# Optimization experiments

Hardware: AMD Instinct MI355X
Metric: run time of the kernel (lower is better)

## Reference

```python
import jax, jax.numpy as jnp
import numpy as np
import math

B, T, C, H = 2, 2048, 1024, 16
D = C // H  # head dim 64

def setup_inputs() -> dict:
    key = jax.random.key(0)
    ks = jax.random.split(key, 3)
    scale = 0.02
    return {
        "x": jax.random.normal(ks[0], (B, T, C), dtype=jnp.float32),
        "W_attn": jax.random.normal(ks[1], (C, 3 * C), dtype=jnp.float32) * scale,
        "b_attn": jnp.zeros((3 * C,), dtype=jnp.float32),
        "W_proj": jax.random.normal(ks[2], (C, C), dtype=jnp.float32) * scale,
        "b_proj": jnp.zeros((C,), dtype=jnp.float32),
    }

def reference(x, W_attn, b_attn, W_proj, b_proj):
    Bb, Tt, Cc = x.shape
    qkv = x @ W_attn + b_attn                       # [B,T,3C]
    q, k, v = jnp.split(qkv, 3, axis=-1)
    # [B,T,C] -> [B,H,T,D]
    def heads(t):
        return t.reshape(Bb, Tt, H, D).transpose(0, 2, 1, 3)
    q, k, v = heads(q), heads(k), heads(v)
    scores = jnp.einsum('bhqd,bhkd->bhqk', q, k) * (1.0 / math.sqrt(D))
    causal = jnp.tril(jnp.ones((Tt, Tt), dtype=bool))
    scores = jnp.where(causal, scores, -jnp.inf)
    attn = jax.nn.softmax(scores, axis=-1)
    out = jnp.einsum('bhqk,bhkd->bhqd', attn, v)    # [B,H,T,D]
    out = out.transpose(0, 2, 1, 3).reshape(Bb, Tt, Cc)
    return out @ W_proj + b_proj
```

## Files before the change

kernel.cpp:

```cpp
#include <hip/hip_runtime.h>

typedef unsigned short u16;
typedef unsigned int u32;
typedef float f32x4 __attribute__((ext_vector_type(4)));
typedef float f32x16 __attribute__((ext_vector_type(16)));
typedef unsigned int u32x4 __attribute__((ext_vector_type(4)));
typedef unsigned int u32x2 __attribute__((ext_vector_type(2)));
typedef unsigned short u16x8 __attribute__((ext_vector_type(8)));
typedef unsigned short u16x4 __attribute__((ext_vector_type(4)));

#define DEV static __device__ __forceinline__

constexpr int BB = 2, TT = 2048, CC = 1024, HH = 16, DD = 64;
constexpr int MDIM = BB * TT;

DEV u16 f2bf(float f) {
  unsigned int u = __builtin_bit_cast(unsigned int, f);
  u += 0x7fffu + ((u >> 16) & 1u);
  return (u16)(u >> 16);
}
DEV float bf2f(u16 h) {
  unsigned int u = ((unsigned int)h) << 16;
  return __builtin_bit_cast(float, u);
}
DEV void async16(const void* g, void* l) {
  __builtin_amdgcn_global_load_lds(
      (const __attribute__((address_space(1))) unsigned int*)g,
      (__attribute__((address_space(3))) unsigned int*)l, 16, 0, 0);
}
DEV void mfma16(f32x4& acc, u32x4 a, u32x4 b) {
  asm volatile("v_mfma_f32_16x16x32_bf16 %0, %1, %2, %0"
               : "+v"(acc)
               : "v"(a), "v"(b));
}
DEV void mfma32(f32x16& acc, u32x4 a, u32x4 b) {
  asm volatile("v_mfma_f32_32x32x16_bf16 %0, %1, %2, %0"
               : "+v"(acc)
               : "v"(a), "v"(b));
}
DEV u32 cvtpk(float lo, float hi) {
  u32 r;
  asm("v_cvt_pk_bf16_f32 %0, %1, %2" : "=v"(r) : "v"(lo), "v"(hi));
  return r;
}
DEV void pswap(u32& a, u32& b) {
#if __has_builtin(__builtin_amdgcn_permlane32_swap)
  u32x2 r = __builtin_amdgcn_permlane32_swap(a, b, false, false);
  a = r.x;
  b = r.y;
#else
  asm volatile("v_permlane32_swap_b32 %0, %1" : "+v"(a), "+v"(b));
#endif
}
DEV float exp2g(float x) {
#if __has_builtin(__builtin_amdgcn_exp2f)
  return __builtin_amdgcn_exp2f(x);
#else
  return exp2f(x);
#endif
}

__global__ void prep_all(const float* __restrict__ x,
                         const float* __restrict__ Wa, const float* __restrict__ Wp,
                         u16* __restrict__ x_bf,
                         u16* __restrict__ Wa_t, u16* __restrict__ Wp_t) {
  __shared__ float tile[32][33];
  int bx = blockIdx.x;
  const int tx = threadIdx.x, ty = threadIdx.y;
  if (bx >= 128) {
    const int cb = (bx - 128) * 32 + blockIdx.y;
    const int i = (cb * 1024 + ty * 32 + tx) * 4;
    f32x4 v = *(const f32x4*)(x + i);
    u16x4 o;
#pragma unroll
    for (int j = 0; j < 4; ++j) o[j] = f2bf(v[j]);
    *(u16x4*)(x_bf + i) = o;
    return;
  }
  const float* in;
  u16* out;
  int Cc;
  if (bx < 96) { in = Wa; out = Wa_t; Cc = 3072; }
  else { bx -= 96; in = Wp; out = Wp_t; Cc = 1024; }
  const int R = 1024;
  const int x0 = bx * 32, y0 = blockIdx.y * 32;
  tile[ty][tx] = in[(size_t)(y0 + ty) * Cc + (x0 + tx)];
  __syncthreads();
  out[(size_t)(x0 + ty) * R + (y0 + tx)] = f2bf(tile[tx][ty]);
}

__global__ __launch_bounds__(512, 2) void gemm_qkv256(
    const u16* __restrict__ A, const u16* __restrict__ Bt,
    const float* __restrict__ bias,
    u16* __restrict__ qw, u16* __restrict__ kw, u16* __restrict__ vw) {
  extern __shared__ char smem[];
  const int K = CC, NT = K / 64;
  const int tid = threadIdx.x;
  const int lane = tid & 63, w = tid >> 6;
  const int g = lane >> 4, c16 = lane & 15;
  const int wm2 = (w >> 2) * 128, wn2 = (w & 3) * 48;

  const int wgid = blockIdx.x;
  const int xcd = wgid & 7, idx = wgid >> 3;
  const int patch = xcd * 2 + (idx >> 4);
  const int q = idx & 15;
  const int bys = (patch & 3) * 4 + (q & 3);
  const int bxs = (patch >> 2) * 4 + (q >> 2);
  const int brow = bys * 256, bcol = bxs * 192;

  const int lrow = lane >> 3;
  const int scol = ((lane & 7) ^ lrow) << 4;
  const int rswz = (c16 & 7) << 4;

  f32x4 acc[8][3];
#pragma unroll
  for (int m = 0; m < 8; ++m)
#pragma unroll
    for (int n = 0; n < 3; ++n) acc[m][n] = f32x4{0.f, 0.f, 0.f, 0.f};

  const size_t ldb = (size_t)K * 2;
  const char* Abase = (const char*)A + (size_t)brow * ldb;
  const char* Bbase = (const char*)Bt + (size_t)bcol * ldb;

  auto STAGE = [&](int kt) {
    const int par = kt & 1;
    char* Adst = smem + par * 32768;
    char* Bdst = smem + 65536 + par * 24576;
    const size_t koff = (size_t)kt * 128;
#pragma unroll
    for (int i = 0; i < 4; ++i) {
      const int c = w * 4 + i;
      const int row = c * 8 + lrow;
      async16(Abase + (size_t)row * ldb + koff + scol, Adst + c * 1024);
    }
#pragma unroll
    for (int i = 0; i < 3; ++i) {
      const int c = w * 3 + i;
      const int row = c * 8 + lrow;
      async16(Bbase + (size_t)row * ldb + koff + scol, Bdst + c * 1024);
    }
  };

  STAGE(0);
  STAGE(1);

  for (int kt = 0; kt < NT; ++kt) {
    const int par = kt & 1;
    if (kt + 1 < NT)
      asm volatile("s_waitcnt vmcnt(7)" ::: "memory");
    else
      asm volatile("s_waitcnt vmcnt(0)" ::: "memory");
    __builtin_amdgcn_sched_barrier(0);
    __builtin_amdgcn_s_barrier();
    __builtin_amdgcn_sched_barrier(0);
    const char* Ap = smem + par * 32768;
    const char* Bp = smem + 65536 + par * 24576;
#pragma unroll
    for (int kc = 0; kc < 2; ++kc) {
      const int cb = (kc * 64 + g * 16) ^ rswz;
      u32x4 af[8], bf[3];
#pragma unroll
      for (int m = 0; m < 8; ++m)
        af[m] = *(const u32x4*)(Ap + (wm2 + m * 16 + c16) * 128 + cb);
#pragma unroll
      for (int n = 0; n < 3; ++n)
        bf[n] = *(const u32x4*)(Bp + (wn2 + n * 16 + c16) * 128 + cb);
      asm volatile("s_waitcnt lgkmcnt(0)" ::: "memory");
      __builtin_amdgcn_sched_barrier(0);
      __builtin_amdgcn_s_setprio(1);
#pragma unroll
      for (int m = 0; m < 8; ++m)
#pragma unroll
        for (int n = 0; n < 3; ++n) mfma16(acc[m][n], af[m], bf[n]);
      __builtin_amdgcn_s_setprio(0);
    }
    __builtin_amdgcn_s_barrier();
    if (kt + 2 < NT) STAGE(kt + 2);
  }

  u16* E = (u16*)smem;
#pragma unroll
  for (int n = 0; n < 3; ++n) {
    const float bv = bias[bcol + wn2 + n * 16 + c16];
#pragma unroll
    for (int m = 0; m < 8; ++m)
#pragma unroll
      for (int r = 0; r < 4; ++r)
        E[(wm2 + m * 16 + g * 4 + r) * 192 + wn2 + n * 16 + c16] =
            f2bf(acc[m][n][r] + bv);
  }
  __syncthreads();
#pragma unroll
  for (int i = 0; i < 12; ++i) {
    const int c = tid + i * 512;
    {
      const int row = c / 24, col8 = (c % 24) * 8;
      const int colg = bcol + col8;
      if (colg < 2048) {
        const int which = colg >> 10, cc = colg & 1023, h = cc >> 6, d = cc & 63;
        const int rowg = brow + row, b = rowg >> 11, t = rowg & (TT - 1);
        u16x8 v8 = *(const u16x8*)&E[row * 192 + col8];
        u16* dst = (which == 0 ? qw : kw) + ((size_t)(b * HH + h) * TT + t) * DD + d;
        *(u16x8*)dst = v8;
      }
    }
    {
      const int col = c % 192, row8 = (c / 192) * 8;
      const int colg = bcol + col;
      if (colg >= 2048) {
        const int cc = colg & 1023, h = cc >> 6, d = cc & 63;
        const int rowg = brow + row8, b = rowg >> 11, t = rowg & (TT - 1);
        u16x8 v8;
#pragma unroll
        for (int j = 0; j < 8; ++j) v8[j] = E[(row8 + j) * 192 + col];
        u16* dst = vw + ((size_t)(b * HH + h) * DD + d) * TT + t;
        *(u16x8*)dst = v8;
      }
    }
  }
}

__global__ __launch_bounds__(256) void gemm_proj(
    const u16* __restrict__ A, const u16* __restrict__ Bt,
    const float* __restrict__ bias, float* __restrict__ outF,
    int M, int N, int K) {
  __shared__ alignas(16) u16 Sh[2][128 * 64];
  u16* Asp = Sh[0];
  u16* Bsp = Sh[1];
  const int tid = threadIdx.x;
  const int lane = tid & 63, w = tid >> 6;
  const int g = lane >> 4, c16 = lane & 15;
  const int wm = (w >> 1) * 64, wn = (w & 1) * 64;

  const int wgid = blockIdx.y * gridDim.x + blockIdx.x;
  const int xcd = wgid & 7, pi = wgid >> 3;
  const int bxs = pi & 7;
  const int bys = 4 * xcd + (pi >> 3);
  const int brow = bys * 128, bcol = bxs * 128;

  const int lrow = lane >> 3;
  const int scol = ((lane & 7) ^ lrow) << 4;
  const int rswz = (c16 & 7) << 4;

  f32x4 acc[4][4];
#pragma unroll
  for (int m = 0; m < 4; ++m)
#pragma unroll
    for (int n = 0; n < 4; ++n) acc[m][n] = f32x4{0.f, 0.f, 0.f, 0.f};

  const size_t ldb = (size_t)K * 2;
  const char* Abase = (const char*)A + (size_t)brow * ldb;
  const char* Bbase = (const char*)Bt + (size_t)bcol * ldb;

  for (int kt = 0; kt < K; kt += 64) {
    __syncthreads();
#pragma unroll
    for (int i = 0; i < 4; ++i) {
      const int chunk = i * 4 + w;
      const int row = chunk * 8 + lrow;
      async16(Abase + (size_t)row * ldb + (size_t)kt * 2 + scol, (char*)Asp + chunk * 1024);
      async16(Bbase + (size_t)row * ldb + (size_t)kt * 2 + scol, (char*)Bsp + chunk * 1024);
    }
    __syncthreads();
#pragma unroll
    for (int kc = 0; kc < 2; ++kc) {
      const int cb = (kc * 64 + g * 16) ^ rswz;
      u32x4 af[4], bf8[4];
#pragma unroll
      for (int m = 0; m < 4; ++m)
        af[m] = *(const u32x4*)((const char*)Asp + (wm + m * 16 + c16) * 128 + cb);
#pragma unroll
      for (int n = 0; n < 4; ++n)
        bf8[n] = *(const u32x4*)((const char*)Bsp + (wn + n * 16 + c16) * 128 + cb);
#pragma unroll
      for (int m = 0; m < 4; ++m)
#pragma unroll
        for (int n = 0; n < 4; ++n) mfma16(acc[m][n], af[m], bf8[n]);
    }
  }

  float* Ef = (float*)&Sh[0][0];
#pragma unroll
  for (int pass = 0; pass < 2; ++pass) {
    __syncthreads();
    if ((wm >> 6) == pass) {
#pragma unroll
      for (int n = 0; n < 4; ++n) {
        const float bv = bias[bcol + wn + n * 16 + c16];
#pragma unroll
        for (int m = 0; m < 4; ++m)
#pragma unroll
          for (int r = 0; r < 4; ++r)
            Ef[(m * 16 + g * 4 + r) * 128 + wn + n * 16 + c16] = acc[m][n][r] + bv;
      }
    }
    __syncthreads();
#pragma unroll
    for (int i = 0; i < 8; ++i) {
      const int chunk = tid + i * 256;
      const int row = chunk >> 5;
      const int c4 = (chunk & 31) * 4;
      f32x4 v4 = *(const f32x4*)&Ef[row * 128 + c4];
      *(f32x4*)&outF[(size_t)(brow + pass * 64 + row) * N + bcol + c4] = v4;
    }
  }
}

__global__ __launch_bounds__(256) void attn_fwd(
    const u16* __restrict__ qw, const u16* __restrict__ kw,
    const u16* __restrict__ vw, u16* __restrict__ ao) {
  extern __shared__ u16 smem_a[];
  const int tid = threadIdx.x;
  const int lane = tid & 63, w = tid >> 6;
  const int ql = lane & 31, half = lane >> 5;
  const int bh = blockIdx.y;
  const int qb = ((bh >> 4) & 1) ? (15 - blockIdx.x) : blockIdx.x;
  const int q0w = qb * 128 + w * 32;
  const int qg = q0w + ql;
  const int lrow = lane >> 3;
  const int scol = ((lane & 7) ^ lrow) << 4;
  const int rswz = (ql & 7) << 4;

  u32x4 qf[4];
  {
    const u16* qrow = qw + ((size_t)bh * TT + qg) * DD;
    const float qs = 0.125f * 1.44269504f;
#pragma unroll
    for (int dwin = 0; dwin < 4; ++dwin) {
      u16x8 u = *(const u16x8*)(qrow + dwin * 16 + half * 8);
      u16x8 s;
#pragma unroll
      for (int j = 0; j < 8; ++j) s[j] = f2bf(bf2f(u[j]) * qs);
      qf[dwin] = __builtin_bit_cast(u32x4, s);
    }
  }

  f32x16 o0, o1;
#pragma unroll
  for (int i = 0; i < 16; ++i) { o0[i] = 0.f; o1[i] = 0.f; }
  float l_run = 0.f;

  const char* kbase = (const char*)kw + ((size_t)bh * TT) * 128;
  const char* vbase = (const char*)vw + ((size_t)bh * DD) * (TT * 2);

  const int nt = 2 * qb + 2;

  auto kptr = [&](int b) { return (char*)(smem_a + (b & 3) * 4096); };
  auto vptr = [&](int b) { return (char*)(smem_a + 16384 + (b & 3) * 4096); };

  auto STAGE = [&](int kt_) {
    if (kt_ >= nt) return;
    const int t0_ = kt_ * 64;
#pragma unroll
    for (int i_ = 0; i_ < 2; ++i_) {
      const int chunk = w * 2 + i_;
      const int row = chunk * 8 + lrow;
      async16(kbase + (size_t)(t0_ + row) * 128 + scol, kptr(kt_) + chunk * 1024);
      async16(vbase + (size_t)row * (TT * 2) + (size_t)t0_ * 2 + scol,
              vptr(kt_) + chunk * 1024);
    }
  };

  auto QK = [&](int kt_, f32x16& sa, f32x16& sb) {
    const char* Kc = kptr(kt_);
#pragma unroll
    for (int i = 0; i < 16; ++i) { sa[i] = 0.f; sb[i] = 0.f; }
    __builtin_amdgcn_s_setprio(1);
#pragma unroll
    for (int dwin = 0; dwin < 4; ++dwin) {
      const int cb = (dwin * 32 + half * 16) ^ rswz;
      u32x4 ak0 = *(const u32x4*)(Kc + (0 + ql) * 128 + cb);
      u32x4 ak1 = *(const u32x4*)(Kc + (32 + ql) * 128 + cb);
      mfma32(sa, ak0, qf[dwin]);
      mfma32(sb, ak1, qf[dwin]);
    }
    __builtin_amdgcn_s_setprio(0);
  };

  auto FINISH = [&](int kt_, f32x16& s0, f32x16& s1) {
    const int t0 = kt_ * 64;
    if (t0 >= q0w + 32) return;
    if (t0 + 63 > q0w) {
      const int kb = t0 + 4 * half - qg;
#pragma unroll
      for (int r = 0; r < 16; ++r) {
        const int ko = (r & 3) + 8 * (r >> 2);
        if (kb + ko > 0) s0[r] = -1e30f;
        if (kb + 32 + ko > 0) s1[r] = -1e30f;
      }
    }
#pragma unroll
    for (int i = 0; i < 16; ++i) {
      s0[i] = exp2g(s0[i]);
      s1[i] = exp2g(s1[i]);
    }
    float a8[8];
#pragma unroll
    for (int i = 0; i < 8; ++i)
      a8[i] = (s0[i] + s0[i + 8]) + (s1[i] + s1[i + 8]);
    float rs = ((a8[0] + a8[1]) + (a8[2] + a8[3])) + ((a8[4] + a8[5]) + (a8[6] + a8[7]));
    rs += __shfl_xor(rs, 32, 64);
    l_run += rs;

    u32x4 pf[4];
#pragma unroll
    for (int win = 0; win < 4; ++win) {
      const int b = (win & 1) * 8;
      u32 w0, w1, w2, w3;
      if (win < 2) {
        w0 = cvtpk(s0[b + 0], s0[b + 1]); w2 = cvtpk(s0[b + 4], s0[b + 5]);
        w1 = cvtpk(s0[b + 2], s0[b + 3]); w3 = cvtpk(s0[b + 6], s0[b + 7]);
      } else {
        w0 = cvtpk(s1[b + 0], s1[b + 1]); w2 = cvtpk(s1[b + 4], s1[b + 5]);
        w1 = cvtpk(s1[b + 2], s1[b + 3]); w3 = cvtpk(s1[b + 6], s1[b + 7]);
      }
      pswap(w0, w2);
      pswap(w1, w3);
      pf[win] = u32x4{w0, w1, w2, w3};
    }
    const char* Vc = vptr(kt_);
    __builtin_amdgcn_s_setprio(1);
#pragma unroll
    for (int win = 0; win < 4; ++win) {
      const int cb = (win * 32 + half * 16) ^ rswz;
      u32x4 av0 = *(const u32x4*)(Vc + (0 + ql) * 128 + cb);
      u32x4 av1 = *(const u32x4*)(Vc + (32 + ql) * 128 + cb);
      mfma32(o0, av0, pf[win]);
      mfma32(o1, av1, pf[win]);
    }
    __builtin_amdgcn_s_setprio(0);
  };

  STAGE(0);
  STAGE(1);
  STAGE(2);
  if (nt >= 3)
    asm volatile("s_waitcnt vmcnt(8)" ::: "memory");
  else
    asm volatile("s_waitcnt vmcnt(4)" ::: "memory");
  __builtin_amdgcn_sched_barrier(0);
  __builtin_amdgcn_s_barrier();
  __builtin_amdgcn_sched_barrier(0);

  f32x16 sA0, sA1, sB0, sB1;
  QK(0, sA0, sA1);

#define BODY(KT, C0, C1, N0, N1)                                          \
  {                                                                       \
    const int kt_b = (KT);                                                \
    if (kt_b + 2 < nt)                                                    \
      asm volatile("s_waitcnt vmcnt(4)" ::: "memory");                    \
    else                                                                  \
      asm volatile("s_waitcnt vmcnt(0)" ::: "memory");                    \
    __builtin_amdgcn_sched_barrier(0);                                    \
    __builtin_amdgcn_s_barrier();                                         \
    __builtin_amdgcn_sched_barrier(0);                                    \
    STAGE(kt_b + 3);                                                      \
    if (kt_b + 1 < nt && (kt_b + 1) * 64 < q0w + 32) QK(kt_b + 1, N0, N1);\
    FINISH(kt_b, C0, C1);                                                 \
  }

  for (int kt2 = 0; kt2 < nt; kt2 += 2) {
    BODY(kt2, sA0, sA1, sB0, sB1);
    BODY(kt2 + 1, sB0, sB1, sA0, sA1);
  }
#undef BODY

  const int b = bh >> 4, h = bh & 15;
  const float inv = 1.f / l_run;
  u16* aorow = ao + ((size_t)(b * TT) + qg) * CC + h * DD;
#pragma unroll
  for (int rg = 0; rg < 4; ++rg) {
    u16x4 t0v, t1v;
#pragma unroll
    for (int j = 0; j < 4; ++j) {
      t0v[j] = f2bf(o0[rg * 4 + j] * inv);
      t1v[j] = f2bf(o1[rg * 4 + j] * inv);
    }
    *(u16x4*)(aorow + 8 * rg + 4 * half) = t0v;
    *(u16x4*)(aorow + 32 + 8 * rg + 4 * half) = t1v;
  }
}

extern "C" void kernel_launch(void* const* d_in, const int* in_sizes, int n_in,
                              void* d_out, int out_size, void* d_ws, size_t ws_size,
                              hipStream_t stream) {
  const float* x  = (const float*)d_in[0];
  const float* Wa = (const float*)d_in[1];
  const float* ba = (const float*)d_in[2];
  const float* Wp = (const float*)d_in[3];
  const float* bp = (const float*)d_in[4];
  float* out = (float*)d_out;

  char* ws = (char*)d_ws;
  const size_t MB = 1ull << 20;
  u16* x_bf = (u16*)(ws);
  u16* ao   = (u16*)(ws);
  u16* Wa_t = (u16*)(ws + 8 * MB);
  u16* Wp_t = (u16*)(ws + 14 * MB);
  u16* q_ws = (u16*)(ws + 16 * MB);
  u16* k_ws = (u16*)(ws + 24 * MB);
  u16* v_ws = (u16*)(ws + 32 * MB);

  static bool attr_set = []() {
    hipFuncSetAttribute((const void*)gemm_qkv256,
                        hipFuncAttributeMaxDynamicSharedMemorySize, 114688);
    hipFuncSetAttribute((const void*)attn_fwd,
                        hipFuncAttributeMaxDynamicSharedMemorySize, 65536);
    return true;
  }();
  (void)attr_set;

  hipLaunchKernelGGL(prep_all, dim3(160, 32), dim3(32, 32), 0, stream,
                     x, Wa, Wp, x_bf, Wa_t, Wp_t);
  hipLaunchKernelGGL(gemm_qkv256, dim3(256), dim3(512), 114688, stream,
                     x_bf, Wa_t, ba, q_ws, k_ws, v_ws);
  hipLaunchKernelGGL(attn_fwd, dim3(TT / 128, BB * HH), dim3(256), 65536, stream,
                     q_ws, k_ws, v_ws, ao);
  hipLaunchKernelGGL(gemm_proj, dim3(CC / 128, MDIM / 128), dim3(256), 0, stream,
                     ao, Wp_t, bp, out, MDIM, CC, CC);
}
```

Baseline: 108.0 us.

## Switch attention to 16x16 MFMA tiles with 8 waves per block

The attention kernel moves from 32x32x16 MFMA with 32 query rows per wave to 16x16x32 MFMA with 16 query rows per wave, and doubles the block to 512 threads (8 waves) covering the same 128 query rows. The P operand is rearranged with ds_bpermute instead of permlane32 swaps, and each wave now stages a single K/V chunk, so the vmcnt thresholds are halved. The aim is more waves per CU and finer causal-mask granularity for better latency hiding. The cost is extra LDS bpermute traffic, more K/V LDS reads per query, and the lower throughput per instruction of the smaller MFMA shape.

```diff
diff --git a/kernel.cpp b/kernel.cpp
--- a/kernel.cpp
+++ b/kernel.cpp
@@ -33,24 +33,10 @@
                : "+v"(acc)
                : "v"(a), "v"(b));
 }
-DEV void mfma32(f32x16& acc, u32x4 a, u32x4 b) {
-  asm volatile("v_mfma_f32_32x32x16_bf16 %0, %1, %2, %0"
-               : "+v"(acc)
-               : "v"(a), "v"(b));
-}
 DEV u32 cvtpk(float lo, float hi) {
   u32 r;
   asm("v_cvt_pk_bf16_f32 %0, %1, %2" : "=v"(r) : "v"(lo), "v"(hi));
   return r;
-}
-DEV void pswap(u32& a, u32& b) {
-#if __has_builtin(__builtin_amdgcn_permlane32_swap)
-  u32x2 r = __builtin_amdgcn_permlane32_swap(a, b, false, false);
-  a = r.x;
-  b = r.y;
-#else
-  asm volatile("v_permlane32_swap_b32 %0, %1" : "+v"(a), "+v"(b));
-#endif
 }
 DEV float exp2g(float x) {
 #if __has_builtin(__builtin_amdgcn_exp2f)
@@ -306,38 +292,40 @@
   }
 }
 
-__global__ __launch_bounds__(256) void attn_fwd(
+__global__ __launch_bounds__(512) void attn_fwd(
     const u16* __restrict__ qw, const u16* __restrict__ kw,
     const u16* __restrict__ vw, u16* __restrict__ ao) {
   extern __shared__ u16 smem_a[];
   const int tid = threadIdx.x;
   const int lane = tid & 63, w = tid >> 6;
-  const int ql = lane & 31, half = lane >> 5;
+  const int q16 = lane & 15, g = lane >> 4;
   const int bh = blockIdx.y;
   const int qb = ((bh >> 4) & 1) ? (15 - blockIdx.x) : blockIdx.x;
-  const int q0w = qb * 128 + w * 32;
-  const int qg = q0w + ql;
+  const int q0w = qb * 128 + w * 16;
+  const int qg = q0w + q16;
   const int lrow = lane >> 3;
   const int scol = ((lane & 7) ^ lrow) << 4;
-  const int rswz = (ql & 7) << 4;
-
-  u32x4 qf[4];
+  const int rswz = (q16 & 7) << 4;
+  const int addr0 = (q16 + 32 * (g & 1)) * 4;
+  const int addr1 = addr0 + 64;
+
+  u32x4 qf[2];
   {
     const u16* qrow = qw + ((size_t)bh * TT + qg) * DD;
     const float qs = 0.125f * 1.44269504f;
 #pragma unroll
-    for (int dwin = 0; dwin < 4; ++dwin) {
-      u16x8 u = *(const u16x8*)(qrow + dwin * 16 + half * 8);
+    for (int kc = 0; kc < 2; ++kc) {
+      u16x8 u = *(const u16x8*)(qrow + kc * 32 + g * 8);
       u16x8 s;
 #pragma unroll
       for (int j = 0; j < 8; ++j) s[j] = f2bf(bf2f(u[j]) * qs);
-      qf[dwin] = __builtin_bit_cast(u32x4, s);
-    }
-  }
-
-  f32x16 o0, o1;
-#pragma unroll
-  for (int i = 0; i < 16; ++i) { o0[i] = 0.f; o1[i] = 0.f; }
+      qf[kc] = __builtin_bit_cast(u32x4, s);
+    }
+  }
+
+  f32x4 o[4];
+#pragma unroll
+  for (int df = 0; df < 4; ++df) o[df] = f32x4{0.f, 0.f, 0.f, 0.f};
   float l_run = 0.f;
 
   const char* kbase = (const char*)kw + ((size_t)bh * TT) * 128;
@@ -351,118 +339,116 @@
   auto STAGE = [&](int kt_) {
     if (kt_ >= nt) return;
     const int t0_ = kt_ * 64;
-#pragma unroll
-    for (int i_ = 0; i_ < 2; ++i_) {
-      const int chunk = w * 2 + i_;
-      const int row = chunk * 8 + lrow;
-      async16(kbase + (size_t)(t0_ + row) * 128 + scol, kptr(kt_) + chunk * 1024);
-      async16(vbase + (size_t)row * (TT * 2) + (size_t)t0_ * 2 + scol,
-              vptr(kt_) + chunk * 1024);
-    }
+    const int row = w * 8 + lrow;
+    async16(kbase + (size_t)(t0_ + row) * 128 + scol, kptr(kt_) + w * 1024);
+    async16(vbase + (size_t)row * (TT * 2) + (size_t)t0_ * 2 + scol,
+            vptr(kt_) + w * 1024);
   };
 
-  auto QK = [&](int kt_, f32x16& sa, f32x16& sb) {
+  auto QK = [&](int kt_, f32x4* sa) {
+#pragma unroll
+    for (int kf = 0; kf < 4; ++kf) sa[kf] = f32x4{0.f, 0.f, 0.f, 0.f};
     const char* Kc = kptr(kt_);
-#pragma unroll
-    for (int i = 0; i < 16; ++i) { sa[i] = 0.f; sb[i] = 0.f; }
     __builtin_amdgcn_s_setprio(1);
 #pragma unroll
-    for (int dwin = 0; dwin < 4; ++dwin) {
-      const int cb = (dwin * 32 + half * 16) ^ rswz;
-      u32x4 ak0 = *(const u32x4*)(Kc + (0 + ql) * 128 + cb);
-      u32x4 ak1 = *(const u32x4*)(Kc + (32 + ql) * 128 + cb);
-      mfma32(sa, ak0, qf[dwin]);
-      mfma32(sb, ak1, qf[dwin]);
+    for (int kc = 0; kc < 2; ++kc) {
+      const int cb = (kc * 64 + g * 16) ^ rswz;
+#pragma unroll
+      for (int kf = 0; kf < 4; ++kf) {
+        u32x4 ak = *(const u32x4*)(Kc + (kf * 16 + q16) * 128 + cb);
+        mfma16(sa[kf], ak, qf[kc]);
+      }
     }
     __builtin_amdgcn_s_setprio(0);
   };
 
-  auto FINISH = [&](int kt_, f32x16& s0, f32x16& s1) {
+  auto FINISH = [&](int kt_, f32x4* s) {
     const int t0 = kt_ * 64;
-    if (t0 >= q0w + 32) return;
+    if (t0 >= q0w + 16) return;
     if (t0 + 63 > q0w) {
-      const int kb = t0 + 4 * half - qg;
-#pragma unroll
-      for (int r = 0; r < 16; ++r) {
-        const int ko = (r & 3) + 8 * (r >> 2);
-        if (kb + ko > 0) s0[r] = -1e30f;
-        if (kb + 32 + ko > 0) s1[r] = -1e30f;
-      }
-    }
-#pragma unroll
-    for (int i = 0; i < 16; ++i) {
-      s0[i] = exp2g(s0[i]);
-      s1[i] = exp2g(s1[i]);
-    }
-    float a8[8];
-#pragma unroll
-    for (int i = 0; i < 8; ++i)
-      a8[i] = (s0[i] + s0[i + 8]) + (s1[i] + s1[i + 8]);
-    float rs = ((a8[0] + a8[1]) + (a8[2] + a8[3])) + ((a8[4] + a8[5]) + (a8[6] + a8[7]));
+      const int kb = t0 + g * 4 - qg;
+#pragma unroll
+      for (int kf = 0; kf < 4; ++kf)
+#pragma unroll
+        for (int r = 0; r < 4; ++r)
+          if (kb + kf * 16 + r > 0) s[kf][r] = -1e30f;
+    }
+#pragma unroll
+    for (int kf = 0; kf < 4; ++kf)
+#pragma unroll
+      for (int r = 0; r < 4; ++r) s[kf][r] = exp2g(s[kf][r]);
+    float rs = ((s[0][0] + s[0][1] + s[0][2] + s[0][3]) +
+                (s[1][0] + s[1][1] + s[1][2] + s[1][3])) +
+               ((s[2][0] + s[2][1] + s[2][2] + s[2][3]) +
+                (s[3][0] + s[3][1] + s[3][2] + s[3][3]));
+    rs += __shfl_xor(rs, 16, 64);
     rs += __shfl_xor(rs, 32, 64);
     l_run += rs;
 
-    u32x4 pf[4];
-#pragma unroll
-    for (int win = 0; win < 4; ++win) {
-      const int b = (win & 1) * 8;
-      u32 w0, w1, w2, w3;
-      if (win < 2) {
-        w0 = cvtpk(s0[b + 0], s0[b + 1]); w2 = cvtpk(s0[b + 4], s0[b + 5]);
-        w1 = cvtpk(s0[b + 2], s0[b + 3]); w3 = cvtpk(s0[b + 6], s0[b + 7]);
-      } else {
-        w0 = cvtpk(s1[b + 0], s1[b + 1]); w2 = cvtpk(s1[b + 4], s1[b + 5]);
-        w1 = cvtpk(s1[b + 2], s1[b + 3]); w3 = cvtpk(s1[b + 6], s1[b + 7]);
+#pragma unroll
+    for (int kc = 0; kc < 2; ++kc) {
+      const u32 A0 = cvtpk(s[2 * kc][0], s[2 * kc][1]);
+      const u32 B0 = cvtpk(s[2 * kc][2], s[2 * kc][3]);
+      const u32 A1 = cvtpk(s[2 * kc + 1][0], s[2 * kc + 1][1]);
+      const u32 B1 = cvtpk(s[2 * kc + 1][2], s[2 * kc + 1][3]);
+      const u32 pA0 = __builtin_amdgcn_ds_bpermute(addr0, A0);
+      const u32 pA1 = __builtin_amdgcn_ds_bpermute(addr0, A1);
+      const u32 pB0 = __builtin_amdgcn_ds_bpermute(addr0, B0);
+      const u32 pB1 = __builtin_amdgcn_ds_bpermute(addr0, B1);
+      const u32 qA0 = __builtin_amdgcn_ds_bpermute(addr1, A0);
+      const u32 qA1 = __builtin_amdgcn_ds_bpermute(addr1, A1);
+      const u32 qB0 = __builtin_amdgcn_ds_bpermute(addr1, B0);
+      const u32 qB1 = __builtin_amdgcn_ds_bpermute(addr1, B1);
+      const bool hi = g >= 2;
+      u32x4 pf;
+      pf.x = hi ? pA1 : pA0;
+      pf.y = hi ? pB1 : pB0;
+      pf.z = hi ? qA1 : qA0;
+      pf.w = hi ? qB1 : qB0;
+      const char* Vc = vptr(kt_);
+      __builtin_amdgcn_s_setprio(1);
+      const int cb = (kc * 64 + g * 16) ^ rswz;
+#pragma unroll
+      for (int df = 0; df < 4; ++df) {
+        u32x4 av = *(const u32x4*)(Vc + (df * 16 + q16) * 128 + cb);
+        mfma16(o[df], av, pf);
       }
-      pswap(w0, w2);
-      pswap(w1, w3);
-      pf[win] = u32x4{w0, w1, w2, w3};
-    }
-    const char* Vc = vptr(kt_);
-    __builtin_amdgcn_s_setprio(1);
-#pragma unroll
-    for (int win = 0; win < 4; ++win) {
-      const int cb = (win * 32 + half * 16) ^ rswz;
-      u32x4 av0 = *(const u32x4*)(Vc + (0 + ql) * 128 + cb);
-      u32x4 av1 = *(const u32x4*)(Vc + (32 + ql) * 128 + cb);
-      mfma32(o0, av0, pf[win]);
-      mfma32(o1, av1, pf[win]);
-    }
-    __builtin_amdgcn_s_setprio(0);
+      __builtin_amdgcn_s_setprio(0);
+    }
   };
 
   STAGE(0);
   STAGE(1);
   STAGE(2);
   if (nt >= 3)
-    asm volatile("s_waitcnt vmcnt(8)" ::: "memory");
+    asm volatile("s_waitcnt vmcnt(4)" ::: "memory");
   else
-    asm volatile("s_waitcnt vmcnt(4)" ::: "memory");
+    asm volatile("s_waitcnt vmcnt(2)" ::: "memory");
   __builtin_amdgcn_sched_barrier(0);
   __builtin_amdgcn_s_barrier();
   __builtin_amdgcn_sched_barrier(0);
 
-  f32x16 sA0, sA1, sB0, sB1;
-  QK(0, sA0, sA1);
-
-#define BODY(KT, C0, C1, N0, N1)                                          \
+  f32x4 sA[4], sB[4];
+  QK(0, sA);
+
+#define BODY(KT, C, N)                                                    \
   {                                                                       \
     const int kt_b = (KT);                                                \
     if (kt_b + 2 < nt)                                                    \
-      asm volatile("s_waitcnt vmcnt(4)" ::: "memory");                    \
+      asm volatile("s_waitcnt vmcnt(2)" ::: "memory");                    \
     else                                                                  \
       asm volatile("s_waitcnt vmcnt(0)" ::: "memory");                    \
     __builtin_amdgcn_sched_barrier(0);                                    \
     __builtin_amdgcn_s_barrier();                                         \
     __builtin_amdgcn_sched_barrier(0);                                    \
     STAGE(kt_b + 3);                                                      \
-    if (kt_b + 1 < nt && (kt_b + 1) * 64 < q0w + 32) QK(kt_b + 1, N0, N1);\
-    FINISH(kt_b, C0, C1);                                                 \
+    if (kt_b + 1 < nt && (kt_b + 1) * 64 < q0w + 16) QK(kt_b + 1, N);     \
+    FINISH(kt_b, C);                                                      \
   }
 
   for (int kt2 = 0; kt2 < nt; kt2 += 2) {
-    BODY(kt2, sA0, sA1, sB0, sB1);
-    BODY(kt2 + 1, sB0, sB1, sA0, sA1);
+    BODY(kt2, sA, sB);
+    BODY(kt2 + 1, sB, sA);
   }
 #undef BODY
 
@@ -470,15 +456,11 @@
   const float inv = 1.f / l_run;
   u16* aorow = ao + ((size_t)(b * TT) + qg) * CC + h * DD;
 #pragma unroll
-  for (int rg = 0; rg < 4; ++rg) {
-    u16x4 t0v, t1v;
-#pragma unroll
-    for (int j = 0; j < 4; ++j) {
-      t0v[j] = f2bf(o0[rg * 4 + j] * inv);
-      t1v[j] = f2bf(o1[rg * 4 + j] * inv);
-    }
-    *(u16x4*)(aorow + 8 * rg + 4 * half) = t0v;
-    *(u16x4*)(aorow + 32 + 8 * rg + 4 * half) = t1v;
+  for (int df = 0; df < 4; ++df) {
+    u16x4 t4;
+#pragma unroll
+    for (int r = 0; r < 4; ++r) t4[r] = f2bf(o[df][r] * inv);
+    *(u16x4*)(aorow + df * 16 + g * 4) = t4;
   }
 }
 
@@ -515,7 +497,7 @@
                      x, Wa, Wp, x_bf, Wa_t, Wp_t);
   hipLaunchKernelGGL(gemm_qkv256, dim3(256), dim3(512), 114688, stream,
                      x_bf, Wa_t, ba, q_ws, k_ws, v_ws);
-  hipLaunchKernelGGL(attn_fwd, dim3(TT / 128, BB * HH), dim3(256), 65536, stream,
+  hipLaunchKernelGGL(attn_fwd, dim3(TT / 128, BB * HH), dim3(512), 65536, stream,
                      q_ws, k_ws, v_ws, ao);
   hipLaunchKernelGGL(gemm_proj, dim3(CC / 128, MDIM / 128), dim3(256), 0, stream,
                      ao, Wp_t, bp, out, MDIM, CC, CC);
```

After: 116.9 us. 8.3% more time.
